# Kernel tuning notes

Measured on AMD Instinct MI355X. Metric: run time of the kernel, lower is better.

The kernel has to match this reference:

```python
import jax, jax.numpy as jnp
import numpy as np

N_HEADS = 4
DIM_HEAD = 32


def setup_inputs() -> dict:
    key = jax.random.key(0)
    k1, k2, k3, k4 = jax.random.split(key, 4)
    x = jax.random.normal(k1, (8, 64, 80, 1024), dtype=jnp.float32)
    # conv_qkv: 1x1 conv, no bias -> weight [3*heads*dim_head, dim_in_out]
    w_qkv = jax.random.normal(k2, (3 * N_HEADS * DIM_HEAD, 64), dtype=jnp.float32) * 0.05
    # conv_out: 1x1 conv with bias -> weight [dim_in_out, heads*dim_head], bias [dim_in_out]
    w_out = jax.random.normal(k3, (64, N_HEADS * DIM_HEAD), dtype=jnp.float32) * 0.05
    b_out = jax.random.normal(k4, (64,), dtype=jnp.float32) * 0.05
    return {"x": x, "w_qkv": w_qkv, "w_out": w_out, "b_out": b_out}


def reference(x, w_qkv, w_out, b_out):
    b, c, h, w = x.shape
    n = h * w
    # 1x1 conv == channel matmul
    qkv = jnp.einsum('bchw,oc->bohw', x, w_qkv)            # [b, 3*heads*dh, h, w]
    qkv = qkv.reshape(b, 3, N_HEADS, DIM_HEAD, n)          # qkv outermost, then heads, then c
    q, k, v = qkv[:, 0], qkv[:, 1], qkv[:, 2]              # each [b, heads, dh, n]
    k = jax.nn.softmax(k, axis=-1)                          # softmax over spatial positions
    context = jnp.einsum('bhdn,bhen->bhde', k, v)          # [b, heads, dh, dh]
    out = jnp.einsum('bhde,bhdn->bhen', context, q)        # [b, heads, dh, n]
    out = out.reshape(b, N_HEADS * DIM_HEAD, h, w)
    return jnp.einsum('bchw,oc->bohw', out, w_out) + b_out[None, :, None, None]
```

## Files before the change

### kernel.cpp

```cpp
#include <hip/hip_runtime.h>
#include <stdint.h>


#define N_POS 81920
#define NT    64
#define TILES 1280

typedef short bf16x8 __attribute__((ext_vector_type(8)));
typedef float f32x4  __attribute__((ext_vector_type(4)));

__device__ __forceinline__ uint32_t packbf(float lo, float hi){
  uint32_t a = __float_as_uint(lo), b = __float_as_uint(hi);
  a = (a + 0x8000u) >> 16;
  b = (b + 0x8000u) & 0xffff0000u;
  return a | b;
}
__device__ __forceinline__ short bf16of(float v){
  return (short)((__float_as_uint(v) + 0x8000u) >> 16);
}

__global__ __launch_bounds__(256, 2) void kernA(
    const float* __restrict__ x, const float* __restrict__ w,
    float* __restrict__ pA, float* __restrict__ pZ, int nch, int tpc)
{
  __shared__ __align__(16) uint16_t xs_cp[64 * 72];
  __shared__ __align__(16) uint16_t xs_pc[64 * 72];
  __shared__ __align__(16) uint16_t es[128 * 72];

  const int t  = threadIdx.x;
  const int wv = t >> 6;
  const int l  = t & 63;
  const int lm = l & 15;
  const int lg = l >> 4;

  const int b  = blockIdx.x / nch;
  const int ch = blockIdx.x % nch;
  const float* xb = x + (size_t)b * 64 * N_POS;

  bf16x8 wkf[8][2];
  #pragma unroll
  for (int ht = 0; ht < 8; ++ht)
    #pragma unroll
    for (int kk = 0; kk < 2; ++kk){
      const float* wp = w + (size_t)(128 + 16*ht + lm) * 64 + 32*kk + 8*lg;
      float4 w0 = *(const float4*)wp;
      float4 w1 = *(const float4*)(wp + 4);
      bf16x8 f;
      f[0]=bf16of(w0.x); f[1]=bf16of(w0.y); f[2]=bf16of(w0.z); f[3]=bf16of(w0.w);
      f[4]=bf16of(w1.x); f[5]=bf16of(w1.y); f[6]=bf16of(w1.z); f[7]=bf16of(w1.w);
      wkf[ht][kk] = f;
    }

  bf16x8 ones;
  #pragma unroll
  for (int j = 0; j < 8; ++j) ones[j] = (short)0x3F80;

  f32x4 acc[2][4], zac[2];
  #pragma unroll
  for (int m = 0; m < 2; ++m){
    zac[m] = (f32x4){0.f,0.f,0.f,0.f};
    #pragma unroll
    for (int n = 0; n < 4; ++n) acc[m][n] = (f32x4){0.f,0.f,0.f,0.f};
  }

  for (int tile = 0; tile < tpc; ++tile){
    const int n0 = (ch * tpc + tile) * NT;
    __syncthreads();

    {
      const int rr = t >> 2, pc = t & 3;
      const float* g = xb + (size_t)rr * N_POS + n0 + 16*pc;
      float4 a0 = *(const float4*)g;
      float4 a1 = *(const float4*)(g + 4);
      float4 a2 = *(const float4*)(g + 8);
      float4 a3 = *(const float4*)(g + 12);
      uint4 v0, v1;
      v0.x = packbf(a0.x,a0.y); v0.y = packbf(a0.z,a0.w);
      v0.z = packbf(a1.x,a1.y); v0.w = packbf(a1.z,a1.w);
      v1.x = packbf(a2.x,a2.y); v1.y = packbf(a2.z,a2.w);
      v1.z = packbf(a3.x,a3.y); v1.w = packbf(a3.z,a3.w);
      *(uint4*)&xs_cp[rr*72 + 16*pc]     = v0;
      *(uint4*)&xs_cp[rr*72 + 16*pc + 8] = v1;
    }
    {
      const int pp = t & 63, c0 = (t >> 6) * 16;
      float v[16];
      #pragma unroll
      for (int i = 0; i < 16; ++i)
        v[i] = xb[(size_t)(c0 + i) * N_POS + n0 + pp];
      uint4 u0, u1;
      u0.x = packbf(v[0],v[1]);   u0.y = packbf(v[2],v[3]);
      u0.z = packbf(v[4],v[5]);   u0.w = packbf(v[6],v[7]);
      u1.x = packbf(v[8],v[9]);   u1.y = packbf(v[10],v[11]);
      u1.z = packbf(v[12],v[13]); u1.w = packbf(v[14],v[15]);
      *(uint4*)&xs_pc[pp*72 + c0]     = u0;
      *(uint4*)&xs_pc[pp*72 + c0 + 8] = u1;
    }
    __syncthreads();

    {
      bf16x8 af0 = *(const bf16x8*)&xs_pc[(16*wv + lm)*72 + 8*lg];
      bf16x8 af1 = *(const bf16x8*)&xs_pc[(16*wv + lm)*72 + 32 + 8*lg];
      #pragma unroll
      for (int ht = 0; ht < 8; ++ht){
        f32x4 s = (f32x4){0.f,0.f,0.f,0.f};
        s = __builtin_amdgcn_mfma_f32_16x16x32_bf16(af0, wkf[ht][0], s, 0,0,0);
        s = __builtin_amdgcn_mfma_f32_16x16x32_bf16(af1, wkf[ht][1], s, 0,0,0);
        float e0 = __expf(s[0]), e1 = __expf(s[1]);
        float e2 = __expf(s[2]), e3 = __expf(s[3]);
        uint2 pk; pk.x = packbf(e0,e1); pk.y = packbf(e2,e3);
        *(uint2*)&es[(16*ht + lm)*72 + 16*wv + 4*lg] = pk;
      }
    }
    __syncthreads();

    #pragma unroll
    for (int kk = 0; kk < 2; ++kk){
      bf16x8 ea[2], xbf[4];
      #pragma unroll
      for (int m = 0; m < 2; ++m)
        ea[m] = *(const bf16x8*)&es[(16*(2*wv+m) + lm)*72 + 32*kk + 8*lg];
      #pragma unroll
      for (int n = 0; n < 4; ++n)
        xbf[n] = *(const bf16x8*)&xs_cp[(16*n + lm)*72 + 32*kk + 8*lg];
      #pragma unroll
      for (int m = 0; m < 2; ++m){
        #pragma unroll
        for (int n = 0; n < 4; ++n)
          acc[m][n] = __builtin_amdgcn_mfma_f32_16x16x32_bf16(ea[m], xbf[n], acc[m][n], 0,0,0);
        zac[m] = __builtin_amdgcn_mfma_f32_16x16x32_bf16(ea[m], ones, zac[m], 0,0,0);
      }
    }
  }

  float* pa = pA + (size_t)blockIdx.x * 8192;
  #pragma unroll
  for (int m = 0; m < 2; ++m){
    const int hd0 = 16*(2*wv + m) + 4*lg;
    #pragma unroll
    for (int n = 0; n < 4; ++n)
      #pragma unroll
      for (int r = 0; r < 4; ++r)
        pa[(size_t)(hd0 + r)*64 + 16*n + lm] = acc[m][n][r];
    if (lm == 0){
      #pragma unroll
      for (int r = 0; r < 4; ++r)
        pZ[(size_t)blockIdx.x * 128 + hd0 + r] = zac[m][r];
    }
  }
}

__global__ __launch_bounds__(256) void kernR1(
    const float* __restrict__ pA, const float* __restrict__ pZ,
    float* __restrict__ Ar, float* __restrict__ Zr, int nch)
{
  const int b = blockIdx.x >> 3, s = blockIdx.x & 7;
  const int off = s * 1024 + threadIdx.x * 4;
  float4 a = make_float4(0.f, 0.f, 0.f, 0.f);
  for (int ch = 0; ch < nch; ++ch){
    float4 v = *(const float4*)&pA[(size_t)(b * nch + ch) * 8192 + off];
    a.x += v.x; a.y += v.y; a.z += v.z; a.w += v.w;
  }
  *(float4*)&Ar[(size_t)b * 8192 + off] = a;
  if (s == 0 && threadIdx.x < 128){
    float z = 0.f;
    for (int ch = 0; ch < nch; ++ch) z += pZ[(size_t)(b * nch + ch) * 128 + threadIdx.x];
    Zr[b * 128 + threadIdx.x] = z;
  }
}

__global__ __launch_bounds__(256) void kernR2(
    const float* __restrict__ Ar, const float* __restrict__ Zr,
    const float* __restrict__ w, float* __restrict__ ctx)
{
  __shared__ float A[128 * 65];
  __shared__ float Z[128];
  const int b = blockIdx.x, t = threadIdx.x;

  #pragma unroll
  for (int k = 0; k < 32; ++k){
    int i = t + 256 * k;
    A[(i >> 6) * 65 + (i & 63)] = Ar[(size_t)b * 8192 + i];
  }
  if (t < 128) Z[t] = Zr[b * 128 + t];
  __syncthreads();

  const int hd = t & 127, h = hd >> 5, e0 = (t >> 7) * 16;
  const float rz = 1.0f / Z[hd];
  for (int je = 0; je < 16; ++je){
    int e = e0 + je;
    const float* wv = w + (size_t)(256 + 32 * h + e) * 64;
    float a = 0.f;
    #pragma unroll
    for (int c = 0; c < 64; ++c) a = fmaf(A[hd * 65 + c], wv[c], a);
    ctx[((size_t)b * 128 + hd) * 32 + e] = a * rz;
  }
}

__global__ __launch_bounds__(256) void kernM(
    const float* __restrict__ ctx, const float* __restrict__ w_qkv,
    const float* __restrict__ w_out, float* __restrict__ M)
{
  __shared__ float cs[128 * 33];
  __shared__ float T[64 * 129];
  const int b = blockIdx.x, t = threadIdx.x;

  #pragma unroll
  for (int k = 0; k < 16; ++k){
    int i = t + 256 * k;
    cs[(i >> 5) * 33 + (i & 31)] = ctx[(size_t)b * 4096 + i];
  }
  __syncthreads();

  const int o = t & 63, g = t >> 6;
  for (int jh = 0; jh < 32; ++jh){
    int hd = 32 * g + jh, h = g;
    const float* wo = w_out + (size_t)o * 128 + 32 * h;
    float a = 0.f;
    #pragma unroll
    for (int e = 0; e < 32; ++e) a = fmaf(wo[e], cs[hd * 33 + e], a);
    T[o * 129 + hd] = a;
  }
  __syncthreads();

  const int c0 = 16 * g;
  float m[16];
  #pragma unroll
  for (int j = 0; j < 16; ++j) m[j] = 0.f;
  for (int hd = 0; hd < 128; ++hd){
    float tv = T[o * 129 + hd];
    const float* wq = w_qkv + (size_t)hd * 64 + c0;
    #pragma unroll
    for (int j = 0; j < 16; ++j) m[j] = fmaf(tv, wq[j], m[j]);
  }
  #pragma unroll
  for (int j = 0; j < 16; ++j) M[(size_t)b * 4096 + o * 64 + c0 + j] = m[j];
}

__global__ __launch_bounds__(256, 2) void kernO(
    const float* __restrict__ x, const float* __restrict__ M,
    const float* __restrict__ b_out, float* __restrict__ out)
{
  __shared__ __align__(16) uint16_t xs[256 * 72];

  const int t  = threadIdx.x;
  const int wv = t >> 6;
  const int l  = t & 63;
  const int lm = l & 15;
  const int lg = l >> 4;

  const int b  = blockIdx.x / 320;
  const int p0 = (blockIdx.x % 320) * 256;
  const float* xb = x + (size_t)b * 64 * N_POS + p0;

  const float* Mb = M + (size_t)b * 4096;
  bf16x8 mb[4][2];
  float bias[4];
  #pragma unroll
  for (int ot = 0; ot < 4; ++ot){
    bias[ot] = b_out[16*ot + lm];
    #pragma unroll
    for (int kk = 0; kk < 2; ++kk){
      const float* mp = Mb + (size_t)(16*ot + lm)*64 + 32*kk + 8*lg;
      float4 m0 = *(const float4*)mp;
      float4 m1 = *(const float4*)(mp + 4);
      bf16x8 f;
      f[0]=bf16of(m0.x); f[1]=bf16of(m0.y); f[2]=bf16of(m0.z); f[3]=bf16of(m0.w);
      f[4]=bf16of(m1.x); f[5]=bf16of(m1.y); f[6]=bf16of(m1.z); f[7]=bf16of(m1.w);
      mb[ot][kk] = f;
    }
  }

  #pragma unroll
  for (int cc = 0; cc < 8; ++cc){
    float v[8];
    #pragma unroll
    for (int j = 0; j < 8; ++j)
      v[j] = xb[(size_t)(8*cc + j) * N_POS + t];
    uint4 u;
    u.x = packbf(v[0],v[1]); u.y = packbf(v[2],v[3]);
    u.z = packbf(v[4],v[5]); u.w = packbf(v[6],v[7]);
    *(uint4*)&xs[t*72 + 8*cc] = u;
  }
  __syncthreads();

  float* ob = out + (size_t)b * 64 * N_POS + p0;

  #pragma unroll
  for (int ip = 0; ip < 4; ++ip){
    const int pt = 4*wv + ip;
    bf16x8 af0 = *(const bf16x8*)&xs[(16*pt + lm)*72 + 8*lg];
    bf16x8 af1 = *(const bf16x8*)&xs[(16*pt + lm)*72 + 32 + 8*lg];
    #pragma unroll
    for (int ot = 0; ot < 4; ++ot){
      f32x4 d = (f32x4){0.f,0.f,0.f,0.f};
      d = __builtin_amdgcn_mfma_f32_16x16x32_bf16(af0, mb[ot][0], d, 0,0,0);
      d = __builtin_amdgcn_mfma_f32_16x16x32_bf16(af1, mb[ot][1], d, 0,0,0);
      float4 st = make_float4(d[0]+bias[ot], d[1]+bias[ot],
                              d[2]+bias[ot], d[3]+bias[ot]);
      *(float4*)&ob[(size_t)(16*ot + lm) * N_POS + 16*pt + 4*lg] = st;
    }
  }
}

extern "C" void kernel_launch(void* const* d_in, const int* in_sizes, int n_in,
                              void* d_out, int out_size, void* d_ws, size_t ws_size,
                              hipStream_t stream)
{
  const float* x     = (const float*)d_in[0];
  const float* w_qkv = (const float*)d_in[1];
  const float* w_out = (const float*)d_in[2];
  const float* b_out = (const float*)d_in[3];
  float* out = (float*)d_out;
  float* ws  = (float*)d_ws;

  static const int cand[] = {64, 40, 32, 20, 16, 10, 8, 5, 4, 2, 1};
  int nch = 1;
  for (int i = 0; i < 11; ++i){
    size_t need = ((size_t)8 * cand[i] * (8192 + 128)
                   + 8 * 8192 + 8 * 128 + (size_t)2 * 8 * 4096) * 4;
    if (need <= ws_size){ nch = cand[i]; break; }
  }
  const int tpc = TILES / nch;

  float* pA  = ws;
  float* pZ  = pA + (size_t)8 * nch * 8192;
  float* Ar  = pZ + (size_t)8 * nch * 128;
  float* Zr  = Ar + (size_t)8 * 8192;
  float* ctx = Zr + (size_t)8 * 128;
  float* M   = ctx + (size_t)8 * 4096;

  kernA<<<8 * nch, 256, 0, stream>>>(x, w_qkv, pA, pZ, nch, tpc);
  kernR1<<<64,     256, 0, stream>>>(pA, pZ, Ar, Zr, nch);
  kernR2<<<8,      256, 0, stream>>>(Ar, Zr, w_qkv, ctx);
  kernM<<<8,       256, 0, stream>>>(ctx, w_qkv, w_out, M);
  kernO<<<2560,    256, 0, stream>>>(x, M, b_out, out);
}
```

Baseline: 207.2 us.

## Double the kernA block to 512 threads, prefetch next tile, fuse ctx/M kernels

The main reduction kernel now runs 512 threads per block, and each of its 8 waves owns one 16-row head-dim slice. It also register-prefetches the next tile's x loads while the current tile's MFMA work runs, to hide global memory latency. The two small post-reduction kernels (context computation and M matrix) are fused into one, which drops a launch and the ctx round-trip through global memory. The cost is higher register pressure from the prefetch buffers, and the launch bounds of (512,4) may force spills.

```diff
diff --git a/kernel.cpp b/kernel.cpp
--- a/kernel.cpp
+++ b/kernel.cpp
@@ -19,7 +19,7 @@
   return (short)((__float_as_uint(v) + 0x8000u) >> 16);
 }
 
-__global__ __launch_bounds__(256, 2) void kernA(
+__global__ __launch_bounds__(512, 4) void kernA(
     const float* __restrict__ x, const float* __restrict__ w,
     float* __restrict__ pA, float* __restrict__ pZ, int nch, int tpc)
 {
@@ -28,7 +28,7 @@
   __shared__ __align__(16) uint16_t es[128 * 72];
 
   const int t  = threadIdx.x;
-  const int wv = t >> 6;
+  const int w8 = t >> 6;
   const int l  = t & 63;
   const int lm = l & 15;
   const int lg = l >> 4;
@@ -37,116 +37,111 @@
   const int ch = blockIdx.x % nch;
   const float* xb = x + (size_t)b * 64 * N_POS;
 
-  bf16x8 wkf[8][2];
-  #pragma unroll
-  for (int ht = 0; ht < 8; ++ht)
+  const int sc  = t >> 3;
+  const int spg = t & 7;
+  const int spp = t & 63;
+  const int scg = t >> 6;
+
+  const int pt  = w8 & 3;
+  const int ht0 = (w8 >> 2) * 4;
+
+  bf16x8 wkf[4][2];
+  #pragma unroll
+  for (int i = 0; i < 4; ++i)
     #pragma unroll
     for (int kk = 0; kk < 2; ++kk){
-      const float* wp = w + (size_t)(128 + 16*ht + lm) * 64 + 32*kk + 8*lg;
+      const float* wp = w + (size_t)(128 + 16*(ht0+i) + lm) * 64 + 32*kk + 8*lg;
       float4 w0 = *(const float4*)wp;
       float4 w1 = *(const float4*)(wp + 4);
       bf16x8 f;
       f[0]=bf16of(w0.x); f[1]=bf16of(w0.y); f[2]=bf16of(w0.z); f[3]=bf16of(w0.w);
       f[4]=bf16of(w1.x); f[5]=bf16of(w1.y); f[6]=bf16of(w1.z); f[7]=bf16of(w1.w);
-      wkf[ht][kk] = f;
+      wkf[i][kk] = f;
     }
 
   bf16x8 ones;
   #pragma unroll
   for (int j = 0; j < 8; ++j) ones[j] = (short)0x3F80;
 
-  f32x4 acc[2][4], zac[2];
-  #pragma unroll
-  for (int m = 0; m < 2; ++m){
-    zac[m] = (f32x4){0.f,0.f,0.f,0.f};
-    #pragma unroll
-    for (int n = 0; n < 4; ++n) acc[m][n] = (f32x4){0.f,0.f,0.f,0.f};
+  f32x4 acc[4], zac;
+  zac = (f32x4){0.f,0.f,0.f,0.f};
+  #pragma unroll
+  for (int n = 0; n < 4; ++n) acc[n] = (f32x4){0.f,0.f,0.f,0.f};
+
+  float4 f0, f1;
+  float v[8];
+  {
+    const int n0 = (ch * tpc) * NT;
+    const float* ga = xb + (size_t)sc * N_POS + n0 + 8*spg;
+    f0 = *(const float4*)ga;
+    f1 = *(const float4*)(ga + 4);
+    const float* gb = xb + (size_t)(8*scg) * N_POS + n0 + spp;
+    #pragma unroll
+    for (int i = 0; i < 8; ++i) v[i] = gb[(size_t)i * N_POS];
   }
 
   for (int tile = 0; tile < tpc; ++tile){
-    const int n0 = (ch * tpc + tile) * NT;
     __syncthreads();
-
     {
-      const int rr = t >> 2, pc = t & 3;
-      const float* g = xb + (size_t)rr * N_POS + n0 + 16*pc;
-      float4 a0 = *(const float4*)g;
-      float4 a1 = *(const float4*)(g + 4);
-      float4 a2 = *(const float4*)(g + 8);
-      float4 a3 = *(const float4*)(g + 12);
-      uint4 v0, v1;
-      v0.x = packbf(a0.x,a0.y); v0.y = packbf(a0.z,a0.w);
-      v0.z = packbf(a1.x,a1.y); v0.w = packbf(a1.z,a1.w);
-      v1.x = packbf(a2.x,a2.y); v1.y = packbf(a2.z,a2.w);
-      v1.z = packbf(a3.x,a3.y); v1.w = packbf(a3.z,a3.w);
-      *(uint4*)&xs_cp[rr*72 + 16*pc]     = v0;
-      *(uint4*)&xs_cp[rr*72 + 16*pc + 8] = v1;
+      uint4 u;
+      u.x = packbf(f0.x,f0.y); u.y = packbf(f0.z,f0.w);
+      u.z = packbf(f1.x,f1.y); u.w = packbf(f1.z,f1.w);
+      *(uint4*)&xs_cp[sc*72 + 8*spg] = u;
+      uint4 u2;
+      u2.x = packbf(v[0],v[1]); u2.y = packbf(v[2],v[3]);
+      u2.z = packbf(v[4],v[5]); u2.w = packbf(v[6],v[7]);
+      *(uint4*)&xs_pc[spp*72 + 8*scg] = u2;
+    }
+    __syncthreads();
+    if (tile + 1 < tpc){
+      const int n1 = (ch * tpc + tile + 1) * NT;
+      const float* ga = xb + (size_t)sc * N_POS + n1 + 8*spg;
+      f0 = *(const float4*)ga;
+      f1 = *(const float4*)(ga + 4);
+      const float* gb = xb + (size_t)(8*scg) * N_POS + n1 + spp;
+      #pragma unroll
+      for (int i = 0; i < 8; ++i) v[i] = gb[(size_t)i * N_POS];
     }
     {
-      const int pp = t & 63, c0 = (t >> 6) * 16;
-      float v[16];
-      #pragma unroll
-      for (int i = 0; i < 16; ++i)
-        v[i] = xb[(size_t)(c0 + i) * N_POS + n0 + pp];
-      uint4 u0, u1;
-      u0.x = packbf(v[0],v[1]);   u0.y = packbf(v[2],v[3]);
-      u0.z = packbf(v[4],v[5]);   u0.w = packbf(v[6],v[7]);
-      u1.x = packbf(v[8],v[9]);   u1.y = packbf(v[10],v[11]);
-      u1.z = packbf(v[12],v[13]); u1.w = packbf(v[14],v[15]);
-      *(uint4*)&xs_pc[pp*72 + c0]     = u0;
-      *(uint4*)&xs_pc[pp*72 + c0 + 8] = u1;
-    }
-    __syncthreads();
-
-    {
-      bf16x8 af0 = *(const bf16x8*)&xs_pc[(16*wv + lm)*72 + 8*lg];
-      bf16x8 af1 = *(const bf16x8*)&xs_pc[(16*wv + lm)*72 + 32 + 8*lg];
-      #pragma unroll
-      for (int ht = 0; ht < 8; ++ht){
+      bf16x8 af0 = *(const bf16x8*)&xs_pc[(16*pt + lm)*72 + 8*lg];
+      bf16x8 af1 = *(const bf16x8*)&xs_pc[(16*pt + lm)*72 + 32 + 8*lg];
+      #pragma unroll
+      for (int i = 0; i < 4; ++i){
         f32x4 s = (f32x4){0.f,0.f,0.f,0.f};
-        s = __builtin_amdgcn_mfma_f32_16x16x32_bf16(af0, wkf[ht][0], s, 0,0,0);
-        s = __builtin_amdgcn_mfma_f32_16x16x32_bf16(af1, wkf[ht][1], s, 0,0,0);
+        s = __builtin_amdgcn_mfma_f32_16x16x32_bf16(af0, wkf[i][0], s, 0,0,0);
+        s = __builtin_amdgcn_mfma_f32_16x16x32_bf16(af1, wkf[i][1], s, 0,0,0);
         float e0 = __expf(s[0]), e1 = __expf(s[1]);
         float e2 = __expf(s[2]), e3 = __expf(s[3]);
         uint2 pk; pk.x = packbf(e0,e1); pk.y = packbf(e2,e3);
-        *(uint2*)&es[(16*ht + lm)*72 + 16*wv + 4*lg] = pk;
+        *(uint2*)&es[(16*(ht0+i) + lm)*72 + 16*pt + 4*lg] = pk;
       }
     }
     __syncthreads();
-
     #pragma unroll
     for (int kk = 0; kk < 2; ++kk){
-      bf16x8 ea[2], xbf[4];
-      #pragma unroll
-      for (int m = 0; m < 2; ++m)
-        ea[m] = *(const bf16x8*)&es[(16*(2*wv+m) + lm)*72 + 32*kk + 8*lg];
+      bf16x8 ea = *(const bf16x8*)&es[(16*w8 + lm)*72 + 32*kk + 8*lg];
+      bf16x8 xbf[4];
       #pragma unroll
       for (int n = 0; n < 4; ++n)
         xbf[n] = *(const bf16x8*)&xs_cp[(16*n + lm)*72 + 32*kk + 8*lg];
       #pragma unroll
-      for (int m = 0; m < 2; ++m){
-        #pragma unroll
-        for (int n = 0; n < 4; ++n)
-          acc[m][n] = __builtin_amdgcn_mfma_f32_16x16x32_bf16(ea[m], xbf[n], acc[m][n], 0,0,0);
-        zac[m] = __builtin_amdgcn_mfma_f32_16x16x32_bf16(ea[m], ones, zac[m], 0,0,0);
-      }
+      for (int n = 0; n < 4; ++n)
+        acc[n] = __builtin_amdgcn_mfma_f32_16x16x32_bf16(ea, xbf[n], acc[n], 0,0,0);
+      zac = __builtin_amdgcn_mfma_f32_16x16x32_bf16(ea, ones, zac, 0,0,0);
     }
   }
 
   float* pa = pA + (size_t)blockIdx.x * 8192;
-  #pragma unroll
-  for (int m = 0; m < 2; ++m){
-    const int hd0 = 16*(2*wv + m) + 4*lg;
-    #pragma unroll
-    for (int n = 0; n < 4; ++n)
-      #pragma unroll
-      for (int r = 0; r < 4; ++r)
-        pa[(size_t)(hd0 + r)*64 + 16*n + lm] = acc[m][n][r];
-    if (lm == 0){
-      #pragma unroll
-      for (int r = 0; r < 4; ++r)
-        pZ[(size_t)blockIdx.x * 128 + hd0 + r] = zac[m][r];
-    }
+  const int hd0 = 16*w8 + 4*lg;
+  #pragma unroll
+  for (int n = 0; n < 4; ++n)
+    #pragma unroll
+    for (int r = 0; r < 4; ++r)
+      pa[(size_t)(hd0 + r)*64 + 16*n + lm] = acc[n][r];
+  if (lm == 0){
+    #pragma unroll
+    for (int r = 0; r < 4; ++r)
+      pZ[(size_t)blockIdx.x * 128 + hd0 + r] = zac[r];
   }
 }
 
@@ -169,12 +164,15 @@
   }
 }
 
-__global__ __launch_bounds__(256) void kernR2(
+__global__ __launch_bounds__(256) void kernCM(
     const float* __restrict__ Ar, const float* __restrict__ Zr,
-    const float* __restrict__ w, float* __restrict__ ctx)
+    const float* __restrict__ w_qkv, const float* __restrict__ w_out,
+    float* __restrict__ M)
 {
   __shared__ float A[128 * 65];
   __shared__ float Z[128];
+  __shared__ float cs[128 * 33];
+  __shared__ float T[64 * 129];
   const int b = blockIdx.x, t = threadIdx.x;
 
   #pragma unroll
@@ -185,37 +183,24 @@
   if (t < 128) Z[t] = Zr[b * 128 + t];
   __syncthreads();
 
-  const int hd = t & 127, h = hd >> 5, e0 = (t >> 7) * 16;
-  const float rz = 1.0f / Z[hd];
-  for (int je = 0; je < 16; ++je){
-    int e = e0 + je;
-    const float* wv = w + (size_t)(256 + 32 * h + e) * 64;
-    float a = 0.f;
-    #pragma unroll
-    for (int c = 0; c < 64; ++c) a = fmaf(A[hd * 65 + c], wv[c], a);
-    ctx[((size_t)b * 128 + hd) * 32 + e] = a * rz;
-  }
-}
-
-__global__ __launch_bounds__(256) void kernM(
-    const float* __restrict__ ctx, const float* __restrict__ w_qkv,
-    const float* __restrict__ w_out, float* __restrict__ M)
-{
-  __shared__ float cs[128 * 33];
-  __shared__ float T[64 * 129];
-  const int b = blockIdx.x, t = threadIdx.x;
-
-  #pragma unroll
-  for (int k = 0; k < 16; ++k){
-    int i = t + 256 * k;
-    cs[(i >> 5) * 33 + (i & 31)] = ctx[(size_t)b * 4096 + i];
+  {
+    const int hd = t & 127, h = hd >> 5, e0 = (t >> 7) * 16;
+    const float rz = 1.0f / Z[hd];
+    for (int je = 0; je < 16; ++je){
+      int e = e0 + je;
+      const float* wv = w_qkv + (size_t)(256 + 32 * h + e) * 64;
+      float a = 0.f;
+      #pragma unroll
+      for (int c = 0; c < 64; ++c) a = fmaf(A[hd * 65 + c], wv[c], a);
+      cs[hd * 33 + e] = a * rz;
+    }
   }
   __syncthreads();
 
   const int o = t & 63, g = t >> 6;
   for (int jh = 0; jh < 32; ++jh){
-    int hd = 32 * g + jh, h = g;
-    const float* wo = w_out + (size_t)o * 128 + 32 * h;
+    int hd = 32 * g + jh;
+    const float* wo = w_out + (size_t)o * 128 + 32 * g;
     float a = 0.f;
     #pragma unroll
     for (int e = 0; e < 32; ++e) a = fmaf(wo[e], cs[hd * 33 + e], a);
@@ -318,7 +303,7 @@
   int nch = 1;
   for (int i = 0; i < 11; ++i){
     size_t need = ((size_t)8 * cand[i] * (8192 + 128)
-                   + 8 * 8192 + 8 * 128 + (size_t)2 * 8 * 4096) * 4;
+                   + 8 * 8192 + 8 * 128 + (size_t)8 * 4096) * 4;
     if (need <= ws_size){ nch = cand[i]; break; }
   }
   const int tpc = TILES / nch;
@@ -327,12 +312,10 @@
   float* pZ  = pA + (size_t)8 * nch * 8192;
   float* Ar  = pZ + (size_t)8 * nch * 128;
   float* Zr  = Ar + (size_t)8 * 8192;
-  float* ctx = Zr + (size_t)8 * 128;
-  float* M   = ctx + (size_t)8 * 4096;
-
-  kernA<<<8 * nch, 256, 0, stream>>>(x, w_qkv, pA, pZ, nch, tpc);
+  float* M   = Zr + (size_t)8 * 128;
+
+  kernA<<<8 * nch, 512, 0, stream>>>(x, w_qkv, pA, pZ, nch, tpc);
   kernR1<<<64,     256, 0, stream>>>(pA, pZ, Ar, Zr, nch);
-  kernR2<<<8,      256, 0, stream>>>(Ar, Zr, w_qkv, ctx);
-  kernM<<<8,       256, 0, stream>>>(ctx, w_qkv, w_out, M);
+  kernCM<<<8,      256, 0, stream>>>(Ar, Zr, w_qkv, w_out, M);
   kernO<<<2560,    256, 0, stream>>>(x, M, b_out, out);
 }
```

Measured after the change: 204.1 us. No clear change (-1.5%).
